# Kernel tuning notes

Hardware: AMD Instinct MI355X
Metric: run time of the kernel (lower is better)

Reference implementation:

```python
import jax, jax.numpy as jnp
import numpy as np

SCALE = 0.125          # feature stride 8
OUT = 7                # roi_align output size
SR = 2                 # sampling_ratio
BBW = (10.0, 10.0, 5.0, 5.0)   # torchvision BoxCoder weights
CLAMP = float(np.log(1000.0 / 16.0))
IMG_H, IMG_W = 800.0, 1088.0


def _bilinear(img, ys, xs):
    # img [C,H,W]; ys,xs [P] -> [C,P]
    C, H, W = img.shape
    y = jnp.clip(ys, 0.0, H - 1.0)
    x = jnp.clip(xs, 0.0, W - 1.0)
    y0 = jnp.floor(y); x0 = jnp.floor(x)
    y0i = y0.astype(jnp.int32); x0i = x0.astype(jnp.int32)
    y1i = jnp.minimum(y0i + 1, H - 1); x1i = jnp.minimum(x0i + 1, W - 1)
    ly = y - y0; lx = x - x0
    flat = img.reshape(C, H * W)
    g = lambda yi, xi: flat[:, yi * W + xi]
    return (g(y0i, x0i) * (1 - ly) * (1 - lx) + g(y0i, x1i) * (1 - ly) * lx
            + g(y1i, x0i) * ly * (1 - lx) + g(y1i, x1i) * ly * lx)


def _roi_align(features, boxes, roi_batch):
    # features [B,C,H,W], boxes [N,4] (image coords), roi_batch [N] -> [N,C,7,7]
    B, C, H, W = features.shape
    P = OUT * SR

    def one(b, box):
        x1, y1, x2, y2 = box[0] * SCALE, box[1] * SCALE, box[2] * SCALE, box[3] * SCALE
        rw = jnp.maximum(x2 - x1, 1.0)
        rh = jnp.maximum(y2 - y1, 1.0)
        bw = rw / OUT; bh = rh / OUT
        off = (jnp.arange(OUT)[:, None] + (jnp.arange(SR)[None, :] + 0.5) / SR).reshape(-1)  # [P]
        ys = y1 + off * bh
        xs = x1 + off * bw
        yy = jnp.repeat(ys, P)   # [P*P], y-major
        xx = jnp.tile(xs, P)
        v = _bilinear(features[b], yy, xx)                   # [C, P*P]
        return v.reshape(C, OUT, SR, OUT, SR).mean(axis=(2, 4))  # avg over samples

    return jax.vmap(one)(roi_batch, boxes)


def _decode(deltas, boxes):
    # deltas [N,K,4], boxes [N,4] -> [N,K,4]
    pw = boxes[:, 2] - boxes[:, 0]
    ph = boxes[:, 3] - boxes[:, 1]
    cx = boxes[:, 0] + 0.5 * pw
    cy = boxes[:, 1] + 0.5 * ph
    dx = deltas[..., 0] / BBW[0]; dy = deltas[..., 1] / BBW[1]
    dw = jnp.minimum(deltas[..., 2] / BBW[2], CLAMP)
    dh = jnp.minimum(deltas[..., 3] / BBW[3], CLAMP)
    pcx = dx * pw[:, None] + cx[:, None]
    pcy = dy * ph[:, None] + cy[:, None]
    pww = jnp.exp(dw) * pw[:, None]
    phh = jnp.exp(dh) * ph[:, None]
    out = jnp.stack([
        jnp.clip(pcx - 0.5 * pww, 0.0, IMG_W),
        jnp.clip(pcy - 0.5 * phh, 0.0, IMG_H),
        jnp.clip(pcx + 0.5 * pww, 0.0, IMG_W),
        jnp.clip(pcy + 0.5 * phh, 0.0, IMG_H),
    ], axis=-1)
    return out


def setup_inputs() -> dict:
    key = jax.random.key(0)
    ks = jax.random.split(key, 12)
    B, C, H, W, N, NC = 2, 256, 100, 136, 1000, 2
    features = jax.random.normal(ks[0], (B, C, H, W), jnp.float32)
    # valid proposal boxes in image coords
    cx = jax.random.uniform(ks[1], (N,)) * IMG_W
    cy = jax.random.uniform(ks[2], (N,)) * IMG_H
    bw = jax.random.uniform(ks[3], (N,)) * 240.0 + 16.0
    bh = jax.random.uniform(ks[4], (N,)) * 240.0 + 16.0
    x1 = jnp.clip(cx - 0.5 * bw, 0.0, IMG_W - 2.0)
    y1 = jnp.clip(cy - 0.5 * bh, 0.0, IMG_H - 2.0)
    x2 = jnp.clip(x1 + bw, x1 + 1.0, IMG_W - 1.0)
    y2 = jnp.clip(y1 + bh, y1 + 1.0, IMG_H - 1.0)
    boxes = jnp.stack([x1, y1, x2, y2], axis=-1).astype(jnp.float32)
    roi_batch = jax.random.randint(ks[5], (N,), 0, B, dtype=jnp.int32)
    D = C * OUT * OUT  # 12544
    HID = 1024
    s = 0.02
    fc1_w = jax.random.normal(ks[6], (D, HID), jnp.float32) * s
    fc1_b = jnp.zeros((HID,), jnp.float32)
    fc2_w = jax.random.normal(ks[7], (HID, HID), jnp.float32) * s
    fc2_b = jnp.zeros((HID,), jnp.float32)
    cls_w = jax.random.normal(ks[8], (HID, NC), jnp.float32) * s
    cls_b = jnp.zeros((NC,), jnp.float32)
    bbox_w = jax.random.normal(ks[9], (HID, NC * 4), jnp.float32) * s
    bbox_b = jnp.zeros((NC * 4,), jnp.float32)
    return {"features": features, "boxes": boxes, "roi_batch": roi_batch,
            "fc1_w": fc1_w, "fc1_b": fc1_b, "fc2_w": fc2_w, "fc2_b": fc2_b,
            "cls_w": cls_w, "cls_b": cls_b, "bbox_w": bbox_w, "bbox_b": bbox_b}


def reference(features, boxes, roi_batch, fc1_w, fc1_b, fc2_w, fc2_b, cls_w, cls_b, bbox_w, bbox_b):
    N = boxes.shape[0]
    feats = _roi_align(features, boxes, roi_batch).reshape(N, -1)  # [N, 12544]
    h = jax.nn.relu(feats @ fc1_w + fc1_b)                         # TwoMLPHead fc6
    h = jax.nn.relu(h @ fc2_w + fc2_b)                             # TwoMLPHead fc7
    scores = jax.nn.softmax(h @ cls_w + cls_b, axis=-1)            # [N, 2]
    deltas = (h @ bbox_w + bbox_b).reshape(N, -1, 4)               # [N, 2, 4]
    dec = _decode(deltas, boxes).reshape(N, -1)                    # [N, 8]
    return jnp.concatenate([dec, scores], axis=-1)                 # [N, 10]
```

## Files before the change

### kernel.cpp

```cpp
#include <hip/hip_runtime.h>
#include <hip/hip_bf16.h>

#define BF16 __hip_bfloat16

typedef __bf16 bf16x8 __attribute__((ext_vector_type(8)));
typedef float floatx4 __attribute__((ext_vector_type(4)));

typedef const __attribute__((address_space(1))) void GV;
typedef __attribute__((address_space(3))) void LV;
#define GLD16(gp, lp) __builtin_amdgcn_global_load_lds((GV*)(gp), (LV*)(lp), 16, 0, 0)

__global__ __launch_bounds__(256) void transpose_all(const float* __restrict__ features,
                                                     const float* __restrict__ fc1_w,
                                                     const float* __restrict__ fc2_w,
                                                     BF16* __restrict__ featT,
                                                     BF16* __restrict__ w1t,
                                                     BF16* __restrict__ w2t) {
    __shared__ float tile[64][33];
    int bid = blockIdx.x;
    const float* ip;
    BF16* op;
    int R, C, cx, cy;
    if (bid < 3400) {
        int z = bid / 1700, r = bid - z * 1700;
        cx = r % 425; cy = r / 425;
        R = 256; C = 13600;
        ip = features + (size_t)z * 256 * 13600;
        op = featT + (size_t)z * 256 * 13600;
    } else if (bid < 9672) {
        int r = bid - 3400;
        cx = r & 31; cy = r >> 5;
        R = 12544; C = 1024;
        ip = fc1_w; op = w1t;
    } else {
        int r = bid - 9672;
        cx = r & 31; cy = r >> 5;
        R = 1024; C = 1024;
        ip = fc2_w; op = w2t;
    }
    int tx = threadIdx.x & 31, ty = threadIdx.x >> 5;
    int r0 = cy << 6, c0 = cx << 5;
#pragma unroll
    for (int i = 0; i < 8; ++i)
        tile[ty + i * 8][tx] = ip[(size_t)(r0 + ty + i * 8) * C + c0 + tx];
    __syncthreads();
#pragma unroll
    for (int i = 0; i < 4; ++i) {
        int c = ty + i * 8;
        BF16 a = __float2bfloat16(tile[tx * 2][c]);
        BF16 b = __float2bfloat16(tile[tx * 2 + 1][c]);
        unsigned int pk = (unsigned int)*(unsigned short*)&a |
                          ((unsigned int)*(unsigned short*)&b << 16);
        *(unsigned int*)(op + (size_t)(c0 + c) * R + r0 + tx * 2) = pk;
    }
}

__global__ __launch_bounds__(256) void roi_align_k(const BF16* __restrict__ featT,
                                                   const float* __restrict__ boxes,
                                                   const int* __restrict__ roi_batch,
                                                   BF16* __restrict__ feats) {
    __shared__ __align__(16) int   s_off[196][4];
    __shared__ __align__(16) float s_w[196][4];
    __shared__ BF16 lbuf[12544];
    int roi = blockIdx.x;
    int t = threadIdx.x;
    BF16* orow = feats + (size_t)roi * 12544;
    if (roi >= 1000) {
        uint4* o4 = (uint4*)orow;
        uint4 z = {0u, 0u, 0u, 0u};
        for (int i = t; i < 1568; i += 256) o4[i] = z;
        return;
    }
    int b = roi_batch[roi];

    if (t < 196) {
        float x1 = boxes[roi * 4 + 0] * 0.125f;
        float y1 = boxes[roi * 4 + 1] * 0.125f;
        float x2 = boxes[roi * 4 + 2] * 0.125f;
        float y2 = boxes[roi * 4 + 3] * 0.125f;
        float bw = fmaxf(x2 - x1, 1.0f) * (1.0f / 7.0f);
        float bh = fmaxf(y2 - y1, 1.0f) * (1.0f / 7.0f);
        int cell = t >> 2, s = t & 3;
        int oy = cell / 7, ox = cell - oy * 7;
        int sy = s >> 1, sx = s & 1;
        float yc = y1 + ((float)oy + ((float)sy + 0.5f) * 0.5f) * bh;
        float xc = x1 + ((float)ox + ((float)sx + 0.5f) * 0.5f) * bw;
        yc = fminf(fmaxf(yc, 0.0f), 99.0f);
        xc = fminf(fmaxf(xc, 0.0f), 135.0f);
        float y0f = floorf(yc), x0f = floorf(xc);
        int y0 = (int)y0f, x0 = (int)x0f;
        int y1i = min(y0 + 1, 99), x1i = min(x0 + 1, 135);
        float ly = yc - y0f, lx = xc - x0f;
        s_w[t][0] = (1.0f - ly) * (1.0f - lx) * 0.25f;
        s_w[t][1] = (1.0f - ly) * lx * 0.25f;
        s_w[t][2] = ly * (1.0f - lx) * 0.25f;
        s_w[t][3] = ly * lx * 0.25f;
        s_off[t][0] = (y0 * 136 + x0) * 256;
        s_off[t][1] = (y0 * 136 + x1i) * 256;
        s_off[t][2] = (y1i * 136 + x0) * 256;
        s_off[t][3] = (y1i * 136 + x1i) * 256;
    }
    __syncthreads();

    int cb = t & 31, g = t >> 5;
    const BF16* fb = featT + (size_t)b * (100 * 136 * 256) + cb * 8;
    int chbase = cb * 8;
    for (int cell = g; cell < 49; cell += 8) {
        float a[8];
#pragma unroll
        for (int j = 0; j < 8; ++j) a[j] = 0.0f;
#pragma unroll
        for (int s = 0; s < 4; ++s) {
            int p = cell * 4 + s;
#pragma unroll
            for (int tap = 0; tap < 4; ++tap) {
                float w = s_w[p][tap];
                bf16x8 v = *(const bf16x8*)(fb + s_off[p][tap]);
#pragma unroll
                for (int j = 0; j < 8; ++j) a[j] += w * (float)v[j];
            }
        }
#pragma unroll
        for (int j = 0; j < 8; ++j)
            lbuf[(chbase + j) * 49 + cell] = __float2bfloat16(a[j]);
    }
    __syncthreads();
    uint4* o4 = (uint4*)orow;
    const uint4* l4 = (const uint4*)lbuf;
    for (int i = t; i < 1568; i += 256) o4[i] = l4[i];
}

__global__ __launch_bounds__(256) void gemm_splitk(const BF16* __restrict__ A,
                                                   const BF16* __restrict__ Bt,
                                                   float* __restrict__ P,
                                                   int K, int chunk) {
    __shared__ char lds[2][2][16384];
    int b = blockIdx.x;
    int L = (b & 7) * (gridDim.x >> 3) + (b >> 3);
    int tn = L & 7, tm = (L >> 3) & 7, s = L >> 6;

    int w = threadIdx.x >> 6, l = threadIdx.x & 63;
    int wm = w & 1, wn = w >> 1;
    int k0 = s * chunk;

    floatx4 acc[4][4];
#pragma unroll
    for (int i = 0; i < 4; ++i)
#pragma unroll
        for (int j = 0; j < 4; ++j) acc[i][j] = (floatx4){0.f, 0.f, 0.f, 0.f};

    const size_t strideA = (size_t)K * 2;
    int r8 = l >> 3;
    int g8 = (l & 7) ^ r8;
    const char* gA = (const char*)A + (size_t)(tm * 128 + w * 32 + r8) * strideA
                     + (size_t)k0 * 2 + (size_t)g8 * 16;
    const char* gB = (const char*)Bt + (size_t)(tn * 128 + w * 32 + r8) * strideA
                     + (size_t)k0 * 2 + (size_t)g8 * 16;
    int lw = w * 4096 + l * 16;

    int c = l & 15, q = l >> 4;
    int xa0 = ((0 * 4 + q) ^ (c & 7)) * 16;
    int xa1 = ((1 * 4 + q) ^ (c & 7)) * 16;
    int abase = (wm * 64 + c) * 128;
    int bbase = (wn * 64 + c) * 128;

    int nIter = chunk >> 6;

#pragma unroll
    for (int i = 0; i < 4; ++i) {
        GLD16(gA + (size_t)(i * 8) * strideA, &lds[0][0][lw + i * 1024]);
        GLD16(gB + (size_t)(i * 8) * strideA, &lds[0][1][lw + i * 1024]);
    }
    __syncthreads();

    for (int kb = 0; kb < nIter; ++kb) {
        int cur = kb & 1;
        if (kb + 1 < nIter) {
            size_t ko = (size_t)(kb + 1) * 128;
#pragma unroll
            for (int i = 0; i < 4; ++i) {
                GLD16(gA + (size_t)(i * 8) * strideA + ko, &lds[cur ^ 1][0][lw + i * 1024]);
                GLD16(gB + (size_t)(i * 8) * strideA + ko, &lds[cur ^ 1][1][lw + i * 1024]);
            }
        }
        const char* bufA = lds[cur][0];
        const char* bufB = lds[cur][1];
#pragma unroll
        for (int kk = 0; kk < 2; ++kk) {
            int xo = kk ? xa1 : xa0;
            bf16x8 af[4], bfr[4];
#pragma unroll
            for (int mi = 0; mi < 4; ++mi) af[mi] = *(const bf16x8*)(bufA + abase + mi * 2048 + xo);
#pragma unroll
            for (int ni = 0; ni < 4; ++ni) bfr[ni] = *(const bf16x8*)(bufB + bbase + ni * 2048 + xo);
#pragma unroll
            for (int mi = 0; mi < 4; ++mi)
#pragma unroll
                for (int ni = 0; ni < 4; ++ni)
                    acc[mi][ni] = __builtin_amdgcn_mfma_f32_16x16x32_bf16(af[mi], bfr[ni], acc[mi][ni], 0, 0, 0);
        }
        __syncthreads();
    }

    size_t base = (size_t)s << 20;
#pragma unroll
    for (int mi = 0; mi < 4; ++mi) {
        int rowG = tm * 128 + wm * 64 + mi * 16 + q * 4;
#pragma unroll
        for (int ni = 0; ni < 4; ++ni) {
            int colG = tn * 128 + wn * 64 + ni * 16 + c;
#pragma unroll
            for (int r = 0; r < 4; ++r)
                P[base + (size_t)(rowG + r) * 1024 + colG] = acc[mi][ni][r];
        }
    }
}

__global__ __launch_bounds__(256) void gemm_fc2(const BF16* __restrict__ A,
                                                const BF16* __restrict__ Bt,
                                                const float* __restrict__ bias,
                                                float* __restrict__ H) {
    __shared__ char lds[2][2][16384];
    int b = blockIdx.x;
    int L = (b & 7) * 8 + (b >> 3);
    int tn = L & 7, tm = L >> 3;

    int w = threadIdx.x >> 6, l = threadIdx.x & 63;
    int wm = w & 1, wn = w >> 1;

    floatx4 acc[4][4];
#pragma unroll
    for (int i = 0; i < 4; ++i)
#pragma unroll
        for (int j = 0; j < 4; ++j) acc[i][j] = (floatx4){0.f, 0.f, 0.f, 0.f};

    const size_t strideA = 2048;
    int r8 = l >> 3;
    int g8 = (l & 7) ^ r8;
    const char* gA = (const char*)A + (size_t)(tm * 128 + w * 32 + r8) * strideA
                     + (size_t)g8 * 16;
    const char* gB = (const char*)Bt + (size_t)(tn * 128 + w * 32 + r8) * strideA
                     + (size_t)g8 * 16;
    int lw = w * 4096 + l * 16;

    int c = l & 15, q = l >> 4;
    int xa0 = ((0 * 4 + q) ^ (c & 7)) * 16;
    int xa1 = ((1 * 4 + q) ^ (c & 7)) * 16;
    int abase = (wm * 64 + c) * 128;
    int bbase = (wn * 64 + c) * 128;

    const int nIter = 16;

#pragma unroll
    for (int i = 0; i < 4; ++i) {
        GLD16(gA + (size_t)(i * 8) * strideA, &lds[0][0][lw + i * 1024]);
        GLD16(gB + (size_t)(i * 8) * strideA, &lds[0][1][lw + i * 1024]);
    }
    __syncthreads();

    for (int kb = 0; kb < nIter; ++kb) {
        int cur = kb & 1;
        if (kb + 1 < nIter) {
            size_t ko = (size_t)(kb + 1) * 128;
#pragma unroll
            for (int i = 0; i < 4; ++i) {
                GLD16(gA + (size_t)(i * 8) * strideA + ko, &lds[cur ^ 1][0][lw + i * 1024]);
                GLD16(gB + (size_t)(i * 8) * strideA + ko, &lds[cur ^ 1][1][lw + i * 1024]);
            }
        }
        const char* bufA = lds[cur][0];
        const char* bufB = lds[cur][1];
#pragma unroll
        for (int kk = 0; kk < 2; ++kk) {
            int xo = kk ? xa1 : xa0;
            bf16x8 af[4], bfr[4];
#pragma unroll
            for (int mi = 0; mi < 4; ++mi) af[mi] = *(const bf16x8*)(bufA + abase + mi * 2048 + xo);
#pragma unroll
            for (int ni = 0; ni < 4; ++ni) bfr[ni] = *(const bf16x8*)(bufB + bbase + ni * 2048 + xo);
#pragma unroll
            for (int mi = 0; mi < 4; ++mi)
#pragma unroll
                for (int ni = 0; ni < 4; ++ni)
                    acc[mi][ni] = __builtin_amdgcn_mfma_f32_16x16x32_bf16(af[mi], bfr[ni], acc[mi][ni], 0, 0, 0);
        }
        __syncthreads();
    }

#pragma unroll
    for (int mi = 0; mi < 4; ++mi) {
        int rowG = tm * 128 + wm * 64 + mi * 16 + q * 4;
#pragma unroll
        for (int ni = 0; ni < 4; ++ni) {
            int colG = tn * 128 + wn * 64 + ni * 16 + c;
            float bv = bias[colG];
#pragma unroll
            for (int r = 0; r < 4; ++r)
                H[(size_t)(rowG + r) * 1024 + colG] = fmaxf(acc[mi][ni][r] + bv, 0.0f);
        }
    }
}

__global__ __launch_bounds__(256) void reduce_k(const float* __restrict__ P,
                                                const float* __restrict__ bias,
                                                BF16* __restrict__ out,
                                                int S) {
    int i = blockIdx.x * 256 + threadIdx.x;
    float a = bias[i & 1023];
    for (int s = 0; s < S; ++s) a += P[((size_t)s << 20) + i];
    a = fmaxf(a, 0.0f);
    out[i] = __float2bfloat16(a);
}

__global__ __launch_bounds__(256) void head_k(const float* __restrict__ H,
                                              const float* __restrict__ cls_w,
                                              const float* __restrict__ cls_b,
                                              const float* __restrict__ bbox_w,
                                              const float* __restrict__ bbox_b,
                                              const float* __restrict__ boxes,
                                              float* __restrict__ out) {
    __shared__ float red[4][10];
    int roi = blockIdx.x;
    int t = threadIdx.x, w = t >> 6, l = t & 63;
    int k4 = t * 4;

    floatx4 h = *(const floatx4*)(H + (size_t)roi * 1024 + k4);

    float acc[10];
#pragma unroll
    for (int j = 0; j < 10; ++j) acc[j] = 0.0f;
    floatx4 c0 = *(const floatx4*)(cls_w + k4 * 2);
    floatx4 c1 = *(const floatx4*)(cls_w + k4 * 2 + 4);
    acc[0] = h.x * c0.x + h.y * c0.z + h.z * c1.x + h.w * c1.z;
    acc[1] = h.x * c0.y + h.y * c0.w + h.z * c1.y + h.w * c1.w;
    const float* bw = bbox_w + k4 * 8;
#pragma unroll
    for (int kk = 0; kk < 4; ++kk) {
        float hv = (kk == 0) ? h.x : (kk == 1) ? h.y : (kk == 2) ? h.z : h.w;
        floatx4 b0 = *(const floatx4*)(bw + kk * 8);
        floatx4 b1 = *(const floatx4*)(bw + kk * 8 + 4);
        acc[2] += hv * b0.x; acc[3] += hv * b0.y; acc[4] += hv * b0.z; acc[5] += hv * b0.w;
        acc[6] += hv * b1.x; acc[7] += hv * b1.y; acc[8] += hv * b1.z; acc[9] += hv * b1.w;
    }
#pragma unroll
    for (int j = 0; j < 10; ++j) {
#pragma unroll
        for (int off = 32; off > 0; off >>= 1) acc[j] += __shfl_down(acc[j], off);
    }
    if (l == 0) {
#pragma unroll
        for (int j = 0; j < 10; ++j) red[w][j] = acc[j];
    }
    __syncthreads();
    if (t == 0) {
        float f[10];
#pragma unroll
        for (int j = 0; j < 10; ++j) f[j] = red[0][j] + red[1][j] + red[2][j] + red[3][j];
        float s0 = f[0] + cls_b[0], s1 = f[1] + cls_b[1];
        float m = fmaxf(s0, s1);
        float e0 = expf(s0 - m), e1 = expf(s1 - m);
        float inv = 1.0f / (e0 + e1);

        float bx1 = boxes[roi * 4 + 0], by1 = boxes[roi * 4 + 1];
        float bx2 = boxes[roi * 4 + 2], by2 = boxes[roi * 4 + 3];
        float pw = bx2 - bx1, ph = by2 - by1;
        float cx = bx1 + 0.5f * pw, cy = by1 + 0.5f * ph;
        const float CLAMPV = 4.135166556742356f;
        float* orow = out + roi * 10;
#pragma unroll
        for (int cl = 0; cl < 2; ++cl) {
            float dx = (f[2 + cl * 4 + 0] + bbox_b[cl * 4 + 0]) * 0.1f;
            float dy = (f[2 + cl * 4 + 1] + bbox_b[cl * 4 + 1]) * 0.1f;
            float dw = fminf((f[2 + cl * 4 + 2] + bbox_b[cl * 4 + 2]) * 0.2f, CLAMPV);
            float dh = fminf((f[2 + cl * 4 + 3] + bbox_b[cl * 4 + 3]) * 0.2f, CLAMPV);
            float pcx = dx * pw + cx, pcy = dy * ph + cy;
            float pww = expf(dw) * pw, phh = expf(dh) * ph;
            orow[cl * 4 + 0] = fminf(fmaxf(pcx - 0.5f * pww, 0.0f), 1088.0f);
            orow[cl * 4 + 1] = fminf(fmaxf(pcy - 0.5f * phh, 0.0f), 800.0f);
            orow[cl * 4 + 2] = fminf(fmaxf(pcx + 0.5f * pww, 0.0f), 1088.0f);
            orow[cl * 4 + 3] = fminf(fmaxf(pcy + 0.5f * phh, 0.0f), 800.0f);
        }
        orow[8] = e0 * inv;
        orow[9] = e1 * inv;
    }
}

extern "C" void kernel_launch(void* const* d_in, const int* in_sizes, int n_in,
                              void* d_out, int out_size, void* d_ws, size_t ws_size,
                              hipStream_t stream) {
    const float* features = (const float*)d_in[0];
    const float* boxes    = (const float*)d_in[1];
    const int*   roi_b    = (const int*)d_in[2];
    const float* fc1_w    = (const float*)d_in[3];
    const float* fc1_b    = (const float*)d_in[4];
    const float* fc2_w    = (const float*)d_in[5];
    const float* fc2_b    = (const float*)d_in[6];
    const float* cls_w    = (const float*)d_in[7];
    const float* cls_b    = (const float*)d_in[8];
    const float* bbox_w   = (const float*)d_in[9];
    const float* bbox_b   = (const float*)d_in[10];
    float* out = (float*)d_out;

    char* ws = (char*)d_ws;
    BF16* featT = (BF16*)(ws + 0);
    BF16* w1t   = (BF16*)(ws + 13926400);
    BF16* w2t   = (BF16*)(ws + 39616512);
    BF16* feats = (BF16*)(ws + 41713664);
    BF16* h1    = (BF16*)(ws + 67403776);
    float* P1   = (float*)(ws + 69500928);
    float* H2   = (float*)(ws + 0);

    int S1 = 7;

    transpose_all<<<10184, 256, 0, stream>>>(features, fc1_w, fc2_w, featT, w1t, w2t);

    roi_align_k<<<1024, 256, 0, stream>>>(featT, boxes, roi_b, feats);

    gemm_splitk<<<64 * S1, 256, 0, stream>>>(feats, w1t, P1, 12544, 12544 / S1);
    reduce_k<<<4096, 256, 0, stream>>>(P1, fc1_b, h1, S1);

    gemm_fc2<<<64, 256, 0, stream>>>(h1, w2t, fc2_b, H2);

    head_k<<<1000, 256, 0, stream>>>(H2, cls_w, cls_b, bbox_w, bbox_b, boxes, out);
}
```

Before: 212.8 us.

## Triple-buffer split-K GEMM LDS staging with explicit vmcnt waits

Converts the split-K GEMM main loop from double to triple buffering in LDS. Two tiles are prefetched ahead, and each iteration waits with a partial vmcnt so only the oldest tile's global-to-LDS loads have to finish, followed by a single barrier instead of two. This is meant to hide more global load latency behind MFMA work. It raises LDS use to 96KB per block, which may cut occupancy, and it relies on hand-written waitcnt ordering being correct.

Result: slower. 217.8 us (+2.3%).

```diff
diff --git a/kernel.cpp b/kernel.cpp
--- a/kernel.cpp
+++ b/kernel.cpp
@@ -130,11 +130,23 @@
     for (int i = t; i < 1568; i += 256) o4[i] = l4[i];
 }
 
+#define STAGE_TILE(kbi, bj)                                                     \
+    do {                                                                        \
+        size_t ko_ = (size_t)(kbi) * 128;                                       \
+        _Pragma("unroll")                                                       \
+        for (int i_ = 0; i_ < 4; ++i_) {                                        \
+            GLD16(gA + (size_t)(i_ * 8) * strideA + ko_,                        \
+                  &lds[bj][0][lw + i_ * 1024]);                                 \
+            GLD16(gB + (size_t)(i_ * 8) * strideA + ko_,                        \
+                  &lds[bj][1][lw + i_ * 1024]);                                 \
+        }                                                                       \
+    } while (0)
+
 __global__ __launch_bounds__(256) void gemm_splitk(const BF16* __restrict__ A,
                                                    const BF16* __restrict__ Bt,
                                                    float* __restrict__ P,
                                                    int K, int chunk) {
-    __shared__ char lds[2][2][16384];
+    __shared__ char lds[3][2][16384];
     int b = blockIdx.x;
     int L = (b & 7) * (gridDim.x >> 3) + (b >> 3);
     int tn = L & 7, tm = (L >> 3) & 7, s = L >> 6;
@@ -166,25 +178,22 @@
 
     int nIter = chunk >> 6;
 
-#pragma unroll
-    for (int i = 0; i < 4; ++i) {
-        GLD16(gA + (size_t)(i * 8) * strideA, &lds[0][0][lw + i * 1024]);
-        GLD16(gB + (size_t)(i * 8) * strideA, &lds[0][1][lw + i * 1024]);
-    }
-    __syncthreads();
-
+    STAGE_TILE(0, 0);
+    if (nIter > 1) STAGE_TILE(1, 1);
+
+    int bi = 0;
+    int sj = 2;
     for (int kb = 0; kb < nIter; ++kb) {
-        int cur = kb & 1;
-        if (kb + 1 < nIter) {
-            size_t ko = (size_t)(kb + 1) * 128;
-#pragma unroll
-            for (int i = 0; i < 4; ++i) {
-                GLD16(gA + (size_t)(i * 8) * strideA + ko, &lds[cur ^ 1][0][lw + i * 1024]);
-                GLD16(gB + (size_t)(i * 8) * strideA + ko, &lds[cur ^ 1][1][lw + i * 1024]);
-            }
-        }
-        const char* bufA = lds[cur][0];
-        const char* bufB = lds[cur][1];
+        if (kb + 1 < nIter) asm volatile("s_waitcnt vmcnt(8)" ::: "memory");
+        else                asm volatile("s_waitcnt vmcnt(0)" ::: "memory");
+        __builtin_amdgcn_sched_barrier(0);
+        __builtin_amdgcn_s_barrier();
+        __builtin_amdgcn_sched_barrier(0);
+
+        if (kb + 2 < nIter) STAGE_TILE(kb + 2, sj);
+
+        const char* bufA = lds[bi][0];
+        const char* bufB = lds[bi][1];
 #pragma unroll
         for (int kk = 0; kk < 2; ++kk) {
             int xo = kk ? xa1 : xa0;
@@ -199,7 +208,8 @@
                 for (int ni = 0; ni < 4; ++ni)
                     acc[mi][ni] = __builtin_amdgcn_mfma_f32_16x16x32_bf16(af[mi], bfr[ni], acc[mi][ni], 0, 0, 0);
         }
-        __syncthreads();
+        bi = (bi == 2) ? 0 : bi + 1;
+        sj = (sj == 2) ? 0 : sj + 1;
     }
 
     size_t base = (size_t)s << 20;
```
